# Kernel optimization log

Measured on AMD Instinct MI355X. Metric: run time of the kernel, lower is better.

The kernel has to match this reference:

```python
import jax, jax.numpy as jnp
import numpy as np

B = 524288          # batch size
C = 64              # continuous dims
D = 8               # categorical dims
NCAT = 6            # categories per dim -> 6**8 = 1679616 total
NB = 21             # ceil(log2(6**8)) binary dims


def setup_inputs() -> dict:
    key = jax.random.key(0)
    k1, k2, k3 = jax.random.split(key, 3)
    inputs_continuous = jax.random.normal(k1, (B, C), dtype=jnp.float32)
    inputs_categorical = jax.random.randint(k2, (B, D), 0, NCAT, dtype=jnp.int32)
    # uniform dequantization noise in (0,1); keep away from 0 so log() is finite
    dequantization_noise = jax.random.uniform(k3, (B, 2 * NB), dtype=jnp.float32,
                                              minval=0.01, maxval=1.0)
    num_per_dim = jnp.full((D,), NCAT, dtype=jnp.int32)
    # category_factors[i] = prod(num_per_dim[:i]) (mixed-radix factors)
    category_factors = jnp.concatenate(
        [jnp.ones((1,), jnp.int32), jnp.cumprod(num_per_dim[:-1])]).astype(jnp.int32)
    binary_mask = (2 ** jnp.arange(NB - 1, -1, -1)).astype(jnp.int32)
    return {
        "inputs_continuous": inputs_continuous,
        "inputs_categorical": inputs_categorical,
        "dequantization_noise": dequantization_noise,
        "category_factors": category_factors,
        "binary_mask": binary_mask,
    }


def reference(inputs_continuous, inputs_categorical, dequantization_noise,
              category_factors, binary_mask):
    b = inputs_categorical.shape[0]
    nb = binary_mask.shape[0]
    # mixed-radix encode categories to a single decimal code: [B]
    decimal_encoded = jnp.sum(category_factors * inputs_categorical, axis=-1)
    # binary encode: [B, nb] bool
    binary_encoded = (decimal_encoded[:, None] & binary_mask) != 0
    # View noise as [B, nb, 2]; torch code gathers/scatters flat indices
    # 2i + (0 if bit else 1) for max slot, 2i + (1 if bit else 0) for min slot.
    view = dequantization_noise.reshape(b, nb, 2)
    v0, v1 = view[..., 0], view[..., 1]
    max_v = jnp.where(binary_encoded, v0, v1)
    min_v = jnp.where(binary_encoded, v1, v0)
    rescaling_log_probs = -jnp.sum(jnp.log(max_v), axis=-1)  # [B]
    new_min = min_v * max_v  # scatter-multiply into the min slots
    n0 = jnp.where(binary_encoded, max_v, new_min)
    n1 = jnp.where(binary_encoded, new_min, max_v)
    noise_out = jnp.stack([n0, n1], axis=-1).reshape(b, 2 * nb)
    out_continuous = jnp.concatenate([inputs_continuous, noise_out], axis=1)
    # uniform dequantizer: log prob of U(0,1) samples is 0
    dequantization_log_probs = jnp.zeros((b,), out_continuous.dtype)
    return out_continuous, dequantization_log_probs - rescaling_log_probs
```

## Files before the change

### kernel.cpp

```cpp
#include <hip/hip_runtime.h>


constexpr int NB = 21;
constexpr int OUT_COLS = 106;
constexpr int PAIR_STRIDE = 216;
constexpr int PAIRS_PER_WAVE = 4;
constexpr int WAVES = 4;
constexpr int ROWS_PER_BLOCK = WAVES * PAIRS_PER_WAVE * 2;

__global__ __launch_bounds__(256) void dequant_fused_kernel(
    const float* __restrict__ cont,
    const int*   __restrict__ cat,
    const float* __restrict__ noise,
    float* __restrict__ out,
    int B)
{
    __shared__ float sbuf[WAVES * PAIRS_PER_WAVE * PAIR_STRIDE];

    const int tid  = threadIdx.x;
    const int wave = tid >> 6;
    const int lane = tid & 63;
    const int half = lane >> 5;
    const int l    = lane & 31;

    const int wrow0 = blockIdx.x * ROWS_PER_BLOCK + wave * (PAIRS_PER_WAVE * 2);

#pragma unroll
    for (int p = 0; p < PAIRS_PER_WAVE; ++p) {
        const int ra = wrow0 + 2 * p;
        if (ra >= B) break;
        float* buf = sbuf + (wave * PAIRS_PER_WAVE + p) * PAIR_STRIDE;

        const int c = 2 * lane;
        const float2 cv =
            *reinterpret_cast<const float2*>(cont + (size_t)ra * 64 + c);

        const int nrow = ra + half;
        float2 nv = make_float2(1.f, 1.f);
        if (l < NB)
            nv = *reinterpret_cast<const float2*>(noise + (size_t)nrow * 42 + 2 * l);

        const int4 a  = *reinterpret_cast<const int4*>(cat + (size_t)nrow * 8);
        const int4 bq = *reinterpret_cast<const int4*>(cat + (size_t)nrow * 8 + 4);
        const int dec = ((((((bq.w * 6 + bq.z) * 6 + bq.y) * 6 + bq.x) * 6
                           + a.w) * 6 + a.z) * 6 + a.y) * 6 + a.x;

        float lg = 0.f;
        float2 o = make_float2(0.f, 0.f);
        if (l < NB) {
            const int   bit  = (dec >> (20 - l)) & 1;
            const float maxv = bit ? nv.x : nv.y;
            const float minv = bit ? nv.y : nv.x;
            lg = __logf(maxv);
            const float nm = minv * maxv;
            o.x = bit ? maxv : nm;
            o.y = bit ? nm : maxv;
        }

        *reinterpret_cast<float2*>(buf + (c < 64 ? c : c + 42)) = cv;
        if (l < NB)
            *reinterpret_cast<float2*>(buf + (half ? 170 : 64) + 2 * l) = o;

        float s = lg;
#pragma unroll
        for (int m = 16; m; m >>= 1) s += __shfl_xor(s, m, 32);
        if (l == 0) out[(size_t)B * OUT_COLS + nrow] = s;

        if (lane < 53) {
            const float4 v = *reinterpret_cast<const float4*>(buf + 4 * lane);
            *reinterpret_cast<float4*>(out + (size_t)ra * OUT_COLS + 4 * lane) = v;
        }
    }
}

extern "C" void kernel_launch(void* const* d_in, const int* in_sizes, int n_in,
                              void* d_out, int out_size, void* d_ws, size_t ws_size,
                              hipStream_t stream) {
    const float* cont  = (const float*)d_in[0];
    const int*   cat   = (const int*)d_in[1];
    const float* noise = (const float*)d_in[2];

    float* out = (float*)d_out;
    const int B = in_sizes[1] / 8;

    const int grid = (B + ROWS_PER_BLOCK - 1) / ROWS_PER_BLOCK;
    dequant_fused_kernel<<<grid, 256, 0, stream>>>(cont, cat, noise, out, B);
}
```

Before: 93.76 us.

## Process eight rows per wave step with float4 nontemporal loads and stores

Restructures the kernel so each wave handles eight consecutive rows at a time instead of two. Continuous and noise data are read as contiguous float4 vectors with nontemporal loads, and the per-pair row index is derived arithmetically. Log terms are summed through shared memory rather than by warp shuffles. The 848-float output tile is written with full-width float4 nontemporal stores, aiming for wider, fully coalesced memory transactions and fewer partial wave accesses. This adds more LDS traffic and assumes B is a multiple of 8 rows.

```diff
diff --git a/kernel.cpp b/kernel.cpp
--- a/kernel.cpp
+++ b/kernel.cpp
@@ -1,74 +1,113 @@
 #include <hip/hip_runtime.h>
 
 
-constexpr int NB = 21;
+typedef float f4 __attribute__((ext_vector_type(4)));
+
 constexpr int OUT_COLS = 106;
-constexpr int PAIR_STRIDE = 216;
-constexpr int PAIRS_PER_WAVE = 4;
+constexpr int OCTS_PER_WAVE = 2;
 constexpr int WAVES = 4;
-constexpr int ROWS_PER_BLOCK = WAVES * PAIRS_PER_WAVE * 2;
+constexpr int ROWS_PER_BLOCK = WAVES * OCTS_PER_WAVE * 8;
+constexpr int OUT_STAGE = 848;
+constexpr int LG_STRIDE = 24;
+constexpr int SLOT = OUT_STAGE + 8 * LG_STRIDE;
 
-__global__ __launch_bounds__(256) void dequant_fused_kernel(
+__global__ __launch_bounds__(256) void dequant_oct_kernel(
     const float* __restrict__ cont,
     const int*   __restrict__ cat,
     const float* __restrict__ noise,
     float* __restrict__ out,
     int B)
 {
-    __shared__ float sbuf[WAVES * PAIRS_PER_WAVE * PAIR_STRIDE];
+    __shared__ __align__(16) float sbuf[WAVES * OCTS_PER_WAVE * SLOT];
 
     const int tid  = threadIdx.x;
     const int wave = tid >> 6;
     const int lane = tid & 63;
-    const int half = lane >> 5;
-    const int l    = lane & 31;
-
-    const int wrow0 = blockIdx.x * ROWS_PER_BLOCK + wave * (PAIRS_PER_WAVE * 2);
+    const int base = blockIdx.x * ROWS_PER_BLOCK + wave * (OCTS_PER_WAVE * 8);
 
 #pragma unroll
-    for (int p = 0; p < PAIRS_PER_WAVE; ++p) {
-        const int ra = wrow0 + 2 * p;
-        if (ra >= B) break;
-        float* buf = sbuf + (wave * PAIRS_PER_WAVE + p) * PAIR_STRIDE;
+    for (int qq = 0; qq < OCTS_PER_WAVE; ++qq) {
+        const int r0 = base + 8 * qq;
+        if (r0 < B) {
+            float* buf = sbuf + (wave * OCTS_PER_WAVE + qq) * SLOT;
+            float* lgb = buf + OUT_STAGE;
 
-        const int c = 2 * lane;
-        const float2 cv =
-            *reinterpret_cast<const float2*>(cont + (size_t)ra * 64 + c);
+            const float* cp = cont + (size_t)r0 * 64;
+            const f4 c0 = __builtin_nontemporal_load(
+                reinterpret_cast<const f4*>(cp) + lane);
+            const f4 c1 = __builtin_nontemporal_load(
+                reinterpret_cast<const f4*>(cp) + 64 + lane);
 
-        const int nrow = ra + half;
-        float2 nv = make_float2(1.f, 1.f);
-        if (l < NB)
-            nv = *reinterpret_cast<const float2*>(noise + (size_t)nrow * 42 + 2 * l);
+            const float* np = noise + (size_t)r0 * 42;
+            f4 n0 = __builtin_nontemporal_load(
+                reinterpret_cast<const f4*>(np) + lane);
+            f4 n1 = {1.f, 1.f, 1.f, 1.f};
+            if (lane < 20)
+                n1 = __builtin_nontemporal_load(
+                    reinterpret_cast<const f4*>(np) + 64 + lane);
 
-        const int4 a  = *reinterpret_cast<const int4*>(cat + (size_t)nrow * 8);
-        const int4 bq = *reinterpret_cast<const int4*>(cat + (size_t)nrow * 8 + 4);
-        const int dec = ((((((bq.w * 6 + bq.z) * 6 + bq.y) * 6 + bq.x) * 6
-                           + a.w) * 6 + a.z) * 6 + a.y) * 6 + a.x;
+            int dec = 0;
+            if (lane < 8) {
+                const int4 a = *reinterpret_cast<const int4*>(cat + (size_t)(r0 + lane) * 8);
+                const int4 b = *reinterpret_cast<const int4*>(cat + (size_t)(r0 + lane) * 8 + 4);
+                dec = ((((((b.w * 6 + b.z) * 6 + b.y) * 6 + b.x) * 6
+                         + a.w) * 6 + a.z) * 6 + a.y) * 6 + a.x;
+            }
 
-        float lg = 0.f;
-        float2 o = make_float2(0.f, 0.f);
-        if (l < NB) {
-            const int   bit  = (dec >> (20 - l)) & 1;
-            const float maxv = bit ? nv.x : nv.y;
-            const float minv = bit ? nv.y : nv.x;
-            lg = __logf(maxv);
-            const float nm = minv * maxv;
-            o.x = bit ? maxv : nm;
-            o.y = bit ? nm : maxv;
-        }
+            auto do_pair = [&](int p, float va, float vb) {
+                const int r = (p * 781) >> 14;
+                const int j = p - 21 * r;
+                const int dr  = __shfl(dec, r);
+                const int bit = (dr >> (20 - j)) & 1;
+                const float mx = bit ? va : vb;
+                const float mn = bit ? vb : va;
+                const float nm = mn * mx;
+                float2 o;
+                o.x = bit ? mx : nm;
+                o.y = bit ? nm : mx;
+                *reinterpret_cast<float2*>(buf + r * OUT_COLS + 64 + 2 * j) = o;
+                lgb[r * LG_STRIDE + j] = __logf(mx);
+            };
+            do_pair(2 * lane,     n0.x, n0.y);
+            do_pair(2 * lane + 1, n0.z, n0.w);
+            if (lane < 20) {
+                do_pair(128 + 2 * lane, n1.x, n1.y);
+                do_pair(129 + 2 * lane, n1.z, n1.w);
+            }
 
-        *reinterpret_cast<float2*>(buf + (c < 64 ? c : c + 42)) = cv;
-        if (l < NB)
-            *reinterpret_cast<float2*>(buf + (half ? 170 : 64) + 2 * l) = o;
+            {
+                const int rr = lane >> 4;
+                const int cc = 4 * (lane & 15);
+                float* d0 = buf + rr * OUT_COLS + cc;
+                *reinterpret_cast<float2*>(d0)     = make_float2(c0.x, c0.y);
+                *reinterpret_cast<float2*>(d0 + 2) = make_float2(c0.z, c0.w);
+                float* d1 = buf + (rr + 4) * OUT_COLS + cc;
+                *reinterpret_cast<float2*>(d1)     = make_float2(c1.x, c1.y);
+                *reinterpret_cast<float2*>(d1 + 2) = make_float2(c1.z, c1.w);
+            }
 
-        float s = lg;
+            if (lane < 8) {
+                const f4* lp = reinterpret_cast<const f4*>(lgb + LG_STRIDE * lane);
+                const f4 a0 = lp[0], a1 = lp[1], a2 = lp[2], a3 = lp[3], a4 = lp[4];
+                const float s =
+                    ((a0.x + a0.y) + (a0.z + a0.w)) + ((a1.x + a1.y) + (a1.z + a1.w)) +
+                    ((a2.x + a2.y) + (a2.z + a2.w)) + ((a3.x + a3.y) + (a3.z + a3.w)) +
+                    ((a4.x + a4.y) + (a4.z + a4.w)) + lgb[LG_STRIDE * lane + 20];
+                out[(size_t)B * OUT_COLS + r0 + lane] = s;
+            }
+
+            float* op = out + (size_t)r0 * OUT_COLS;
 #pragma unroll
-        for (int m = 16; m; m >>= 1) s += __shfl_xor(s, m, 32);
-        if (l == 0) out[(size_t)B * OUT_COLS + nrow] = s;
-
-        if (lane < 53) {
-            const float4 v = *reinterpret_cast<const float4*>(buf + 4 * lane);
-            *reinterpret_cast<float4*>(out + (size_t)ra * OUT_COLS + 4 * lane) = v;
+            for (int s4 = 0; s4 < 3; ++s4) {
+                const f4 v = *reinterpret_cast<const f4*>(buf + s4 * 256 + 4 * lane);
+                __builtin_nontemporal_store(
+                    v, reinterpret_cast<f4*>(op + s4 * 256) + lane);
+            }
+            if (lane < 20) {
+                const f4 v = *reinterpret_cast<const f4*>(buf + 768 + 4 * lane);
+                __builtin_nontemporal_store(
+                    v, reinterpret_cast<f4*>(op + 768) + lane);
+            }
         }
     }
 }
@@ -84,5 +123,5 @@
     const int B = in_sizes[1] / 8;
 
     const int grid = (B + ROWS_PER_BLOCK - 1) / ROWS_PER_BLOCK;
-    dequant_fused_kernel<<<grid, 256, 0, stream>>>(cont, cat, noise, out, B);
+    dequant_oct_kernel<<<grid, 256, 0, stream>>>(cont, cat, noise, out, B);
 }
```

Result: faster. 79.49 us (-15.2%).
